# Optimization experiments

Hardware: AMD Instinct MI355X
Metric: run time of the kernel (lower is better)

## Reference

```python
import jax, jax.numpy as jnp
import numpy as np

LOSS_WEIGHT = 1.0
RADIUS = 1
DILATION = 2

def _mind_shift_indices():
    # six-neighbourhood offsets in a 3x3x3 kernel (as in torch code)
    six = np.array([[0, 1, 1], [1, 1, 0], [1, 0, 1], [1, 1, 2], [2, 1, 1], [1, 2, 1]])
    dist = ((six[:, None, :] - six[None, :, :]) ** 2).sum(-1)
    x, y = np.meshgrid(np.arange(6), np.arange(6), indexing='ij')
    mask = ((x > y) & (dist == 2)).reshape(-1)
    idx1 = np.repeat(six, 6, axis=0)[mask]
    idx2 = np.tile(six, (6, 1))[mask]
    return idx1, idx2

_IDX1, _IDX2 = _mind_shift_indices()

def _shifted(padded, idx, d, D, H, W):
    # one-hot dilated conv == static slice of replication-padded volume
    outs = [padded[:, :, a * d:a * d + D, b * d:b * d + H, c * d:c * d + W]
            for (a, b, c) in idx]
    return jnp.concatenate(outs, axis=1)  # (N, 12, D, H, W)

def mind_ssc(img, radius=RADIUS, dilation=DILATION):
    N, C, D, H, W = img.shape
    p = dilation
    padded = jnp.pad(img, ((0, 0), (0, 0), (p, p), (p, p), (p, p)), mode='edge')
    diff2 = (_shifted(padded, _IDX1, dilation, D, H, W)
             - _shifted(padded, _IDX2, dilation, D, H, W)) ** 2
    r = radius
    k = 2 * r + 1
    diff2p = jnp.pad(diff2, ((0, 0), (0, 0), (r, r), (r, r), (r, r)), mode='edge')
    ssd = jax.lax.reduce_window(diff2p, 0.0, jax.lax.add,
                                (1, 1, k, k, k), (1, 1, 1, 1, 1), 'VALID') / (k ** 3)
    mind = ssd - jnp.min(ssd, axis=1, keepdims=True)
    mind_var = jnp.mean(mind, axis=1, keepdims=True)
    m = jax.lax.stop_gradient(jnp.mean(mind_var))  # torch uses .item() -> detached
    mind_var = jnp.clip(mind_var, m * 0.001, m * 1000.0)
    return jnp.exp(-mind / mind_var)

def setup_inputs() -> dict:
    key = jax.random.key(0)
    k1, k2 = jax.random.split(key)
    shape = (2, 1, 128, 128, 128)
    predict = jax.random.normal(k1, shape, dtype=jnp.float32)
    target = jax.random.normal(k2, shape, dtype=jnp.float32)
    return {"predict": predict, "target": target}

def reference(predict, target):
    loss = jnp.mean((mind_ssc(predict) - mind_ssc(target)) ** 2)
    return loss * LOSS_WEIGHT
```

## Files before the change

kernel.cpp:

```cpp
#include <hip/hip_runtime.h>


#define DIM 128
#define HW (128 * 128)
#define DHW (128 * 128 * 128)
#define NVOX (2 * DHW)
#define LOSS_COUNT (2.0 * 12.0 * DHW)

#define TS   16
#define SY   18
#define NSP  (SY * TS)
#define CHZ  16
#define PSTR 7

typedef float f4 __attribute__((ext_vector_type(4)));
typedef float f2 __attribute__((ext_vector_type(2)));

__device__ __forceinline__ int clampi(int v) {
    v = v < 0 ? 0 : v;
    return v > 127 ? 127 : v;
}

__device__ __forceinline__ unsigned fkey(float f) {
    unsigned u = __float_as_uint(f);
    return (u & 0x80000000u) ? ~u : (u | 0x80000000u);
}
__device__ __forceinline__ float fdec(unsigned k) {
    unsigned u = (k & 0x80000000u) ? (k ^ 0x80000000u) : ~k;
    return __uint_as_float(u);
}

__device__ __forceinline__ void block_reduce_atomic(float v, double* dst) {
#pragma unroll
    for (int off = 32; off > 0; off >>= 1)
        v += __shfl_down(v, off, 64);
    __shared__ float red[4];
    int lane = threadIdx.x & 63;
    int wid  = threadIdx.x >> 6;
    if (lane == 0) red[wid] = v;
    __syncthreads();
    if (threadIdx.x == 0) {
        double t = (double)red[0] + (double)red[1] + (double)red[2] + (double)red[3];
        atomicAdd(dst, t);
    }
    __syncthreads();
}

__device__ __forceinline__ void block_minmax_atomic(float mnp, float mxp,
                                                    float mnt, float mxt,
                                                    unsigned* keys) {
#pragma unroll
    for (int off = 32; off > 0; off >>= 1) {
        mnp = fminf(mnp, __shfl_down(mnp, off, 64));
        mxp = fmaxf(mxp, __shfl_down(mxp, off, 64));
        mnt = fminf(mnt, __shfl_down(mnt, off, 64));
        mxt = fmaxf(mxt, __shfl_down(mxt, off, 64));
    }
    __shared__ float r[4][4];
    int lane = threadIdx.x & 63, wid = threadIdx.x >> 6;
    if (lane == 0) { r[wid][0] = mnp; r[wid][1] = mxp; r[wid][2] = mnt; r[wid][3] = mxt; }
    __syncthreads();
    if (threadIdx.x == 0) {
        float a = fminf(fminf(r[0][0], r[1][0]), fminf(r[2][0], r[3][0]));
        float b = fmaxf(fmaxf(r[0][1], r[1][1]), fmaxf(r[2][1], r[3][1]));
        float c = fminf(fminf(r[0][2], r[1][2]), fminf(r[2][2], r[3][2]));
        float d = fmaxf(fmaxf(r[0][3], r[1][3]), fmaxf(r[2][3], r[3][3]));
        atomicMin(&keys[0], fkey(a));
        atomicMax(&keys[1], fkey(b));
        atomicMin(&keys[2], fkey(c));
        atomicMax(&keys[3], fkey(d));
    }
    __syncthreads();
}

struct SPos {
    int y0, ym, yp;
    int cx[3], cm[3], cp[3];
    int woff;
};

__device__ __forceinline__ SPos make_spos(int p, int y0t, int x0t, int stride) {
    SPos q;
    int py = p >> 4, px = p & 15;
    int gy = clampi(y0t - 1 + py);
    int gx = x0t + px;
    q.y0 = gy * DIM; q.ym = clampi(gy - 2) * DIM; q.yp = clampi(gy + 2) * DIM;
#pragma unroll
    for (int wx = 0; wx < 3; ++wx) {
        int c = clampi(gx + wx - 1);
        q.cx[wx] = c;
        q.cm[wx] = clampi(c - 2);
        q.cp[wx] = clampi(c + 2);
    }
    q.woff = p * stride;
    return q;
}


__device__ __forceinline__ void stage_pair(const float* __restrict__ ip,
                                           const float* __restrict__ tp,
                                           int zm, int zc, int zp,
                                           const SPos& q, f4* __restrict__ X) {
    f2 acc[12];
#pragma unroll
    for (int c = 0; c < 12; ++c) acc[c] = (f2)0.0f;
#pragma unroll
    for (int wx = 0; wx < 3; ++wx) {
        int o0 = zm + q.y0 + q.cx[wx];
        int o1 = zc + q.y0 + q.cm[wx];
        int o2 = zc + q.ym + q.cx[wx];
        int o3 = zc + q.y0 + q.cp[wx];
        int o4 = zp + q.y0 + q.cx[wx];
        int o5 = zc + q.yp + q.cx[wx];
        f2 s0 = {ip[o0], tp[o0]};
        f2 s1 = {ip[o1], tp[o1]};
        f2 s2 = {ip[o2], tp[o2]};
        f2 s3 = {ip[o3], tp[o3]};
        f2 s4 = {ip[o4], tp[o4]};
        f2 s5 = {ip[o5], tp[o5]};
        f2 d;
        d = s1 - s0; acc[0]  += d * d;
        d = s2 - s0; acc[1]  += d * d;
        d = s2 - s1; acc[2]  += d * d;
        d = s3 - s0; acc[3]  += d * d;
        d = s3 - s2; acc[4]  += d * d;
        d = s4 - s1; acc[5]  += d * d;
        d = s4 - s2; acc[6]  += d * d;
        d = s4 - s3; acc[7]  += d * d;
        d = s5 - s0; acc[8]  += d * d;
        d = s5 - s1; acc[9]  += d * d;
        d = s5 - s3; acc[10] += d * d;
        d = s5 - s4; acc[11] += d * d;
    }
#pragma unroll
    for (int k = 0; k < 6; ++k) {
        f4 w;
        w.x = acc[2 * k].x;     w.y = acc[2 * k].y;
        w.z = acc[2 * k + 1].x; w.w = acc[2 * k + 1].y;
        X[q.woff + k] = w;
    }
}

__device__ __forceinline__ void box3y_pair(const f4* __restrict__ X,
                                           int ty, int tx, f4 q[6]) {
    int b0 = ((ty + 0) * TS + tx) * PSTR;
    int b1 = ((ty + 1) * TS + tx) * PSTR;
    int b2 = ((ty + 2) * TS + tx) * PSTR;
#pragma unroll
    for (int k = 0; k < 6; ++k)
        q[k] = X[b0 + k] + X[b1 + k] + X[b2 + k];
}

__global__ __launch_bounds__(256, 4) void fused_kernel(const float* __restrict__ pred,
                                                       const float* __restrict__ targ,
                                                       double* __restrict__ acc,
                                                       unsigned* __restrict__ keys) {
    __shared__ f4 X[NSP * PSTR];
    const int t = threadIdx.x;
    const int tile = blockIdx.x & 63, n = blockIdx.x >> 6;
    const int x0t = (tile & 7) * TS, y0t = (tile >> 3) * TS;
    const int z0 = blockIdx.y * CHZ;
    const float* ip = pred + (size_t)n * DHW;
    const float* tp = targ + (size_t)n * DHW;

    SPos pa = make_spos(t, y0t, x0t, PSTR);
    const bool hasB = (t + 256) < NSP;
    SPos pb = make_spos(hasB ? (t + 256) : 0, y0t, x0t, PSTR);

    const int ty = t >> 4, tx = t & 15;

    f4 A[6], B[6];
#pragma unroll
    for (int k = 0; k < 6; ++k) { A[k] = (f4)0.0f; B[k] = (f4)0.0f; }

    float vsump = 0.0f, vsumt = 0.0f, lsum = 0.0f;
    float locmnp = 1e30f, locmxp = -1e30f, locmnt = 1e30f, locmxt = -1e30f;

    for (int tz = z0 - 1; tz <= z0 + CHZ; ++tz) {
        int zq = clampi(tz);
        int zc = zq * HW, zm = clampi(zq - 2) * HW, zp = clampi(zq + 2) * HW;
        stage_pair(ip, tp, zm, zc, zp, pa, X);
        if (hasB) stage_pair(ip, tp, zm, zc, zp, pb, X);
        __syncthreads();

        f4 q[6];
        box3y_pair(X, ty, tx, q);
        __syncthreads();

        int ze = tz - 1;
        if (ze >= z0) {
            f4 v[6];
#pragma unroll
            for (int k = 0; k < 6; ++k) v[k] = A[k] + q[k];

            float mnp = v[0][0], mnt = v[0][1];
            float smp = 0.0f, smt = 0.0f;
#pragma unroll
            for (int c = 0; c < 12; ++c) {
                float pv = v[c >> 1][(c & 1) * 2];
                float tv = v[c >> 1][(c & 1) * 2 + 1];
                mnp = fminf(mnp, pv); smp += pv;
                mnt = fminf(mnt, tv); smt += tv;
            }
            float varp = smp * (1.0f / 12.0f) - mnp;
            float vart = smt * (1.0f / 12.0f) - mnt;
            vsump += varp; vsumt += vart;
            locmnp = fminf(locmnp, varp); locmxp = fmaxf(locmxp, varp);
            locmnt = fminf(locmnt, vart); locmxt = fmaxf(locmxt, vart);

            float invp = -1.0f / varp;
            float invt = -1.0f / vart;
            float la = 0.0f;
#pragma unroll
            for (int c = 0; c < 12; ++c) {
                float pv = v[c >> 1][(c & 1) * 2];
                float tv = v[c >> 1][(c & 1) * 2 + 1];
                float ep = __expf((pv - mnp) * invp);
                float et = __expf((tv - mnt) * invt);
                float dd = ep - et;
                la += dd * dd;
            }
            lsum += la;
        }
#pragma unroll
        for (int k = 0; k < 6; ++k) { A[k] = B[k] + q[k]; B[k] = q[k]; }
    }

    block_reduce_atomic(vsump, &acc[0]);
    block_reduce_atomic(vsumt, &acc[1]);
    block_reduce_atomic(lsum,  &acc[2]);
    block_minmax_atomic(locmnp, locmxp, locmnt, locmxt, keys);
}


__global__ void init_kernel(double* __restrict__ acc, unsigned* __restrict__ keys) {
    acc[0] = 0.0; acc[1] = 0.0; acc[2] = 0.0; acc[3] = 0.0;
    keys[0] = 0xFFFFFFFFu; keys[1] = 0u;
    keys[2] = 0xFFFFFFFFu; keys[3] = 0u;
    keys[4] = 0u;
}

__global__ void flag_kernel(const double* __restrict__ acc, unsigned* __restrict__ keys) {
    float m_p = (float)(acc[0] * (1.0 / (double)NVOX));
    float m_t = (float)(acc[1] * (1.0 / (double)NVOX));
    float mnp = fdec(keys[0]), mxp = fdec(keys[1]);
    float mnt = fdec(keys[2]), mxt = fdec(keys[3]);
    bool clean = (mnp >= m_p * 0.001f) && (mxp <= m_p * 1000.0f) &&
                 (mnt >= m_t * 0.001f) && (mxt <= m_t * 1000.0f);
    keys[4] = clean ? 0u : 1u;
}

__device__ __forceinline__ void stage_xsum(const float* __restrict__ im,
                                           int zm, int zc, int zp,
                                           const SPos& q, f4* __restrict__ P) {
    f4 a = (f4)0.0f, b = (f4)0.0f, c = (f4)0.0f;
#pragma unroll
    for (int wx = 0; wx < 3; ++wx) {
        float s0 = im[zm + q.y0 + q.cx[wx]];
        float s1 = im[zc + q.y0 + q.cm[wx]];
        float s2 = im[zc + q.ym + q.cx[wx]];
        float s3 = im[zc + q.y0 + q.cp[wx]];
        float s4 = im[zp + q.y0 + q.cx[wx]];
        float s5 = im[zc + q.yp + q.cx[wx]];
        float d;
        d = s1 - s0; a.x += d * d;
        d = s2 - s0; a.y += d * d;
        d = s2 - s1; a.z += d * d;
        d = s3 - s0; a.w += d * d;
        d = s3 - s2; b.x += d * d;
        d = s4 - s1; b.y += d * d;
        d = s4 - s2; b.z += d * d;
        d = s4 - s3; b.w += d * d;
        d = s5 - s0; c.x += d * d;
        d = s5 - s1; c.y += d * d;
        d = s5 - s3; c.z += d * d;
        d = s5 - s4; c.w += d * d;
    }
    P[q.woff + 0] = a;
    P[q.woff + 1] = b;
    P[q.woff + 2] = c;
}

__device__ __forceinline__ void box3y(const f4* __restrict__ P,
                                      int ty, int tx, f4 q[3]) {
    int base = (ty * TS + tx) * 3;
#pragma unroll
    for (int k = 0; k < 3; ++k)
        q[k] = P[base + k] + P[base + TS * 3 + k] + P[base + 2 * TS * 3 + k];
}

__device__ __forceinline__ float min12(const f4 v[3]) {
    float mn = v[0][0];
#pragma unroll
    for (int i = 0; i < 4; ++i)
        mn = fminf(mn, fminf(v[0][i], fminf(v[1][i], v[2][i])));
    return mn;
}
__device__ __forceinline__ float sum12(const f4 v[3]) {
    float sm = 0.0f;
#pragma unroll
    for (int i = 0; i < 4; ++i)
        sm += v[0][i] + v[1][i] + v[2][i];
    return sm;
}

__global__ __launch_bounds__(256, 4) void loss_kernel(const float* __restrict__ pred,
                                                      const float* __restrict__ targ,
                                                      const double* __restrict__ acc,
                                                      const unsigned* __restrict__ keys,
                                                      double* __restrict__ loss_sum) {
    if (keys[4] == 0u) return;

    __shared__ f4 Xp[NSP * 3];
    __shared__ f4 Xt[NSP * 3];
    const int t = threadIdx.x;
    const int tile = blockIdx.x & 63, n = blockIdx.x >> 6;
    const int x0t = (tile & 7) * TS, y0t = (tile >> 3) * TS;
    const int z0 = blockIdx.y * CHZ;
    const float* ip = pred + (size_t)n * DHW;
    const float* tp = targ + (size_t)n * DHW;

    const float m_p = (float)(acc[0] * (1.0 / (double)NVOX));
    const float m_t = (float)(acc[1] * (1.0 / (double)NVOX));

    SPos pa = make_spos(t, y0t, x0t, 3);
    const bool hasB = (t + 256) < NSP;
    SPos pb = make_spos(hasB ? (t + 256) : 0, y0t, x0t, 3);

    const int ty = t >> 4, tx = t & 15;

    f4 Ap[3], Bp[3], At[3], Bt[3];
#pragma unroll
    for (int q = 0; q < 3; ++q) {
        Ap[q] = (f4)0.0f; Bp[q] = (f4)0.0f;
        At[q] = (f4)0.0f; Bt[q] = (f4)0.0f;
    }
    float lsum = 0.0f;

    for (int tz = z0 - 1; tz <= z0 + CHZ; ++tz) {
        int zq = clampi(tz);
        int zc = zq * HW, zm = clampi(zq - 2) * HW, zp = clampi(zq + 2) * HW;
        stage_xsum(ip, zm, zc, zp, pa, Xp);
        stage_xsum(tp, zm, zc, zp, pa, Xt);
        if (hasB) {
            stage_xsum(ip, zm, zc, zp, pb, Xp);
            stage_xsum(tp, zm, zc, zp, pb, Xt);
        }
        __syncthreads();

        f4 qp[3], qt[3];
        box3y(Xp, ty, tx, qp);
        box3y(Xt, ty, tx, qt);
        __syncthreads();

        int ze = tz - 1;
        if (ze >= z0) {
            f4 vp[3], vt[3];
#pragma unroll
            for (int q = 0; q < 3; ++q) {
                vp[q] = Ap[q] + qp[q];
                vt[q] = At[q] + qt[q];
            }
            float mnp = min12(vp), smp = sum12(vp);
            float mnt = min12(vt), smt = sum12(vt);
            float varp = smp * (1.0f / 12.0f) - mnp;
            varp = fminf(fmaxf(varp, m_p * 0.001f), m_p * 1000.0f);
            float invp = -1.0f / varp;
            float vart = smt * (1.0f / 12.0f) - mnt;
            vart = fminf(fmaxf(vart, m_t * 0.001f), m_t * 1000.0f);
            float invt = -1.0f / vart;

            float a = 0.0f;
#pragma unroll
            for (int q = 0; q < 3; ++q)
#pragma unroll
                for (int i = 0; i < 4; ++i) {
                    float ep = __expf((vp[q][i] - mnp) * invp);
                    float et = __expf((vt[q][i] - mnt) * invt);
                    float dd = ep - et;
                    a += dd * dd;
                }
            lsum += a;
        }
#pragma unroll
        for (int q = 0; q < 3; ++q) {
            Ap[q] = Bp[q] + qp[q]; Bp[q] = qp[q];
            At[q] = Bt[q] + qt[q]; Bt[q] = qt[q];
        }
    }

    block_reduce_atomic(lsum, loss_sum);
}

__global__ void finalize_kernel(const double* __restrict__ acc,
                                const unsigned* __restrict__ keys,
                                float* __restrict__ out) {
    double l = (keys[4] == 0u) ? acc[2] : acc[3];
    out[0] = (float)(l * (1.0 / LOSS_COUNT));
}

extern "C" void kernel_launch(void* const* d_in, const int* in_sizes, int n_in,
                              void* d_out, int out_size, void* d_ws, size_t ws_size,
                              hipStream_t stream) {
    const float* pred = (const float*)d_in[0];
    const float* targ = (const float*)d_in[1];
    float* out = (float*)d_out;
    double* acc = (double*)d_ws;
    unsigned* keys = (unsigned*)((char*)d_ws + 64);

    dim3 block(256);
    dim3 grid(128, 8);

    init_kernel<<<1, 1, 0, stream>>>(acc, keys);
    fused_kernel<<<grid, block, 0, stream>>>(pred, targ, acc, keys);
    flag_kernel<<<1, 1, 0, stream>>>(acc, keys);
    loss_kernel<<<grid, block, 0, stream>>>(pred, targ, acc, keys, &acc[3]);
    finalize_kernel<<<1, 1, 0, stream>>>(acc, keys, out);
}
```

Baseline: 167.0 us.

## Fold init, flag and finalize kernels into memset and loss kernel

```diff
diff --git a/kernel.cpp b/kernel.cpp
--- a/kernel.cpp
+++ b/kernel.cpp
@@ -12,9 +12,11 @@
 #define NSP  (SY * TS)
 #define CHZ  16
 #define PSTR 7
+#define NBLK 1024
 
 typedef float f4 __attribute__((ext_vector_type(4)));
 typedef float f2 __attribute__((ext_vector_type(2)));
+
 
 __device__ __forceinline__ int clampi(int v) {
     v = v < 0 ? 0 : v;
@@ -65,10 +67,10 @@
         float b = fmaxf(fmaxf(r[0][1], r[1][1]), fmaxf(r[2][1], r[3][1]));
         float c = fminf(fminf(r[0][2], r[1][2]), fminf(r[2][2], r[3][2]));
         float d = fmaxf(fmaxf(r[0][3], r[1][3]), fmaxf(r[2][3], r[3][3]));
-        atomicMin(&keys[0], fkey(a));
-        atomicMax(&keys[1], fkey(b));
-        atomicMin(&keys[2], fkey(c));
-        atomicMax(&keys[3], fkey(d));
+        atomicMax(&keys[0], ~fkey(a));
+        atomicMax(&keys[1],  fkey(b));
+        atomicMax(&keys[2], ~fkey(c));
+        atomicMax(&keys[3],  fkey(d));
     }
     __syncthreads();
 }
@@ -96,22 +98,23 @@
     return q;
 }
 
-
 __device__ __forceinline__ void stage_pair(const float* __restrict__ ip,
                                            const float* __restrict__ tp,
                                            int zm, int zc, int zp,
                                            const SPos& q, f4* __restrict__ X) {
+    const int r0 = zm + q.y0, r1 = zc + q.y0, r2 = zc + q.ym;
+    const int r3 = zc + q.yp, r4 = zp + q.y0;
     f2 acc[12];
 #pragma unroll
     for (int c = 0; c < 12; ++c) acc[c] = (f2)0.0f;
 #pragma unroll
     for (int wx = 0; wx < 3; ++wx) {
-        int o0 = zm + q.y0 + q.cx[wx];
-        int o1 = zc + q.y0 + q.cm[wx];
-        int o2 = zc + q.ym + q.cx[wx];
-        int o3 = zc + q.y0 + q.cp[wx];
-        int o4 = zp + q.y0 + q.cx[wx];
-        int o5 = zc + q.yp + q.cx[wx];
+        int o0 = r0 + q.cx[wx];
+        int o1 = r1 + q.cm[wx];
+        int o2 = r2 + q.cx[wx];
+        int o3 = r1 + q.cp[wx];
+        int o4 = r4 + q.cx[wx];
+        int o5 = r3 + q.cx[wx];
         f2 s0 = {ip[o0], tp[o0]};
         f2 s1 = {ip[o1], tp[o1]};
         f2 s2 = {ip[o2], tp[o2]};
@@ -151,117 +154,20 @@
         q[k] = X[b0 + k] + X[b1 + k] + X[b2 + k];
 }
 
-__global__ __launch_bounds__(256, 4) void fused_kernel(const float* __restrict__ pred,
-                                                       const float* __restrict__ targ,
-                                                       double* __restrict__ acc,
-                                                       unsigned* __restrict__ keys) {
-    __shared__ f4 X[NSP * PSTR];
-    const int t = threadIdx.x;
-    const int tile = blockIdx.x & 63, n = blockIdx.x >> 6;
-    const int x0t = (tile & 7) * TS, y0t = (tile >> 3) * TS;
-    const int z0 = blockIdx.y * CHZ;
-    const float* ip = pred + (size_t)n * DHW;
-    const float* tp = targ + (size_t)n * DHW;
-
-    SPos pa = make_spos(t, y0t, x0t, PSTR);
-    const bool hasB = (t + 256) < NSP;
-    SPos pb = make_spos(hasB ? (t + 256) : 0, y0t, x0t, PSTR);
-
-    const int ty = t >> 4, tx = t & 15;
-
-    f4 A[6], B[6];
-#pragma unroll
-    for (int k = 0; k < 6; ++k) { A[k] = (f4)0.0f; B[k] = (f4)0.0f; }
-
-    float vsump = 0.0f, vsumt = 0.0f, lsum = 0.0f;
-    float locmnp = 1e30f, locmxp = -1e30f, locmnt = 1e30f, locmxt = -1e30f;
-
-    for (int tz = z0 - 1; tz <= z0 + CHZ; ++tz) {
-        int zq = clampi(tz);
-        int zc = zq * HW, zm = clampi(zq - 2) * HW, zp = clampi(zq + 2) * HW;
-        stage_pair(ip, tp, zm, zc, zp, pa, X);
-        if (hasB) stage_pair(ip, tp, zm, zc, zp, pb, X);
-        __syncthreads();
-
-        f4 q[6];
-        box3y_pair(X, ty, tx, q);
-        __syncthreads();
-
-        int ze = tz - 1;
-        if (ze >= z0) {
-            f4 v[6];
-#pragma unroll
-            for (int k = 0; k < 6; ++k) v[k] = A[k] + q[k];
-
-            float mnp = v[0][0], mnt = v[0][1];
-            float smp = 0.0f, smt = 0.0f;
-#pragma unroll
-            for (int c = 0; c < 12; ++c) {
-                float pv = v[c >> 1][(c & 1) * 2];
-                float tv = v[c >> 1][(c & 1) * 2 + 1];
-                mnp = fminf(mnp, pv); smp += pv;
-                mnt = fminf(mnt, tv); smt += tv;
-            }
-            float varp = smp * (1.0f / 12.0f) - mnp;
-            float vart = smt * (1.0f / 12.0f) - mnt;
-            vsump += varp; vsumt += vart;
-            locmnp = fminf(locmnp, varp); locmxp = fmaxf(locmxp, varp);
-            locmnt = fminf(locmnt, vart); locmxt = fmaxf(locmxt, vart);
-
-            float invp = -1.0f / varp;
-            float invt = -1.0f / vart;
-            float la = 0.0f;
-#pragma unroll
-            for (int c = 0; c < 12; ++c) {
-                float pv = v[c >> 1][(c & 1) * 2];
-                float tv = v[c >> 1][(c & 1) * 2 + 1];
-                float ep = __expf((pv - mnp) * invp);
-                float et = __expf((tv - mnt) * invt);
-                float dd = ep - et;
-                la += dd * dd;
-            }
-            lsum += la;
-        }
-#pragma unroll
-        for (int k = 0; k < 6; ++k) { A[k] = B[k] + q[k]; B[k] = q[k]; }
-    }
-
-    block_reduce_atomic(vsump, &acc[0]);
-    block_reduce_atomic(vsumt, &acc[1]);
-    block_reduce_atomic(lsum,  &acc[2]);
-    block_minmax_atomic(locmnp, locmxp, locmnt, locmxt, keys);
-}
-
-
-__global__ void init_kernel(double* __restrict__ acc, unsigned* __restrict__ keys) {
-    acc[0] = 0.0; acc[1] = 0.0; acc[2] = 0.0; acc[3] = 0.0;
-    keys[0] = 0xFFFFFFFFu; keys[1] = 0u;
-    keys[2] = 0xFFFFFFFFu; keys[3] = 0u;
-    keys[4] = 0u;
-}
-
-__global__ void flag_kernel(const double* __restrict__ acc, unsigned* __restrict__ keys) {
-    float m_p = (float)(acc[0] * (1.0 / (double)NVOX));
-    float m_t = (float)(acc[1] * (1.0 / (double)NVOX));
-    float mnp = fdec(keys[0]), mxp = fdec(keys[1]);
-    float mnt = fdec(keys[2]), mxt = fdec(keys[3]);
-    bool clean = (mnp >= m_p * 0.001f) && (mxp <= m_p * 1000.0f) &&
-                 (mnt >= m_t * 0.001f) && (mxt <= m_t * 1000.0f);
-    keys[4] = clean ? 0u : 1u;
-}
-
 __device__ __forceinline__ void stage_xsum(const float* __restrict__ im,
                                            int zm, int zc, int zp,
                                            const SPos& q, f4* __restrict__ P) {
+    const int r0 = zm + q.y0, r1 = zc + q.y0, r2 = zc + q.ym;
+    const int r3 = zc + q.yp, r4 = zp + q.y0;
     f4 a = (f4)0.0f, b = (f4)0.0f, c = (f4)0.0f;
 #pragma unroll
     for (int wx = 0; wx < 3; ++wx) {
-        float s0 = im[zm + q.y0 + q.cx[wx]];
-        float s1 = im[zc + q.y0 + q.cm[wx]];
-        float s2 = im[zc + q.ym + q.cx[wx]];
-        float s3 = im[zc + q.y0 + q.cp[wx]];
-        float s4 = im[zp + q.y0 + q.cx[wx]];
-        float s5 = im[zc + q.yp + q.cx[wx]];
+        float s0 = im[r0 + q.cx[wx]];
+        float s1 = im[r1 + q.cm[wx]];
+        float s2 = im[r2 + q.cx[wx]];
+        float s3 = im[r1 + q.cp[wx]];
+        float s4 = im[r4 + q.cx[wx]];
+        float s5 = im[r3 + q.cx[wx]];
         float d;
         d = s1 - s0; a.x += d * d;
         d = s2 - s0; a.y += d * d;
@@ -304,15 +210,13 @@
     return sm;
 }
 
-__global__ __launch_bounds__(256, 4) void loss_kernel(const float* __restrict__ pred,
-                                                      const float* __restrict__ targ,
-                                                      const double* __restrict__ acc,
-                                                      const unsigned* __restrict__ keys,
-                                                      double* __restrict__ loss_sum) {
-    if (keys[4] == 0u) return;
-
-    __shared__ f4 Xp[NSP * 3];
-    __shared__ f4 Xt[NSP * 3];
+
+__global__ __launch_bounds__(256, 4) void fused_kernel(const float* __restrict__ pred,
+                                                       const float* __restrict__ targ,
+                                                       double* __restrict__ acc,
+                                                       unsigned* __restrict__ keys) {
+    __shared__ f4 X[NSP * PSTR];
+
     const int t = threadIdx.x;
     const int tile = blockIdx.x & 63, n = blockIdx.x >> 6;
     const int x0t = (tile & 7) * TS, y0t = (tile >> 3) * TS;
@@ -320,13 +224,112 @@
     const float* ip = pred + (size_t)n * DHW;
     const float* tp = targ + (size_t)n * DHW;
 
-    const float m_p = (float)(acc[0] * (1.0 / (double)NVOX));
-    const float m_t = (float)(acc[1] * (1.0 / (double)NVOX));
+    SPos pa = make_spos(t, y0t, x0t, PSTR);
+    const bool hasB = (t + 256) < NSP;
+    SPos pb = make_spos(hasB ? (t + 256) : 0, y0t, x0t, PSTR);
+    const int ty = t >> 4, tx = t & 15;
+
+    f4 A[6], B[6];
+#pragma unroll
+    for (int k = 0; k < 6; ++k) { A[k] = (f4)0.0f; B[k] = (f4)0.0f; }
+
+    float vsump = 0.0f, vsumt = 0.0f, lsum = 0.0f;
+    float locmnp = 1e30f, locmxp = -1e30f, locmnt = 1e30f, locmxt = -1e30f;
+
+    for (int tz = z0 - 1; tz <= z0 + CHZ; ++tz) {
+        int zq = clampi(tz);
+        int zc = zq * HW, zm = clampi(zq - 2) * HW, zp = clampi(zq + 2) * HW;
+        stage_pair(ip, tp, zm, zc, zp, pa, X);
+        if (hasB) stage_pair(ip, tp, zm, zc, zp, pb, X);
+        __syncthreads();
+
+        f4 q[6];
+        box3y_pair(X, ty, tx, q);
+        __syncthreads();
+
+        int ze = tz - 1;
+        if (ze >= z0) {
+            f4 v[6];
+#pragma unroll
+            for (int k = 0; k < 6; ++k) v[k] = A[k] + q[k];
+
+            f2 sm2 = (f2)0.0f;
+            float mnp = v[0][0], mnt = v[0][1];
+#pragma unroll
+            for (int k = 0; k < 6; ++k) {
+                f2 a = {v[k].x, v[k].y};
+                f2 b = {v[k].z, v[k].w};
+                sm2 += a + b;
+                mnp = fminf(mnp, fminf(v[k].x, v[k].z));
+                mnt = fminf(mnt, fminf(v[k].y, v[k].w));
+            }
+            f2 mn2 = {mnp, mnt};
+            f2 var2 = sm2 * (1.0f / 12.0f) - mn2;
+            vsump += var2.x; vsumt += var2.y;
+            locmnp = fminf(locmnp, var2.x); locmxp = fmaxf(locmxp, var2.x);
+            locmnt = fminf(locmnt, var2.y); locmxt = fmaxf(locmxt, var2.y);
+
+            f2 inv2 = {-1.0f / var2.x, -1.0f / var2.y};
+            float la = 0.0f;
+#pragma unroll
+            for (int k = 0; k < 6; ++k) {
+                f2 a = ({ f2 u = {v[k].x, v[k].y}; (u - mn2) * inv2; });
+                f2 b = ({ f2 u = {v[k].z, v[k].w}; (u - mn2) * inv2; });
+                float d0 = __expf(a.x) - __expf(a.y);
+                float d1 = __expf(b.x) - __expf(b.y);
+                la += d0 * d0 + d1 * d1;
+            }
+            lsum += la;
+        }
+#pragma unroll
+        for (int k = 0; k < 6; ++k) { A[k] = B[k] + q[k]; B[k] = q[k]; }
+    }
+
+    block_reduce_atomic(vsump, &acc[0]);
+    block_reduce_atomic(vsumt, &acc[1]);
+    block_reduce_atomic(lsum,  &acc[2]);
+    block_minmax_atomic(locmnp, locmxp, locmnt, locmxt, keys);
+}
+
+
+__global__ __launch_bounds__(256, 4) void loss_kernel(const float* __restrict__ pred,
+                                                      const float* __restrict__ targ,
+                                                      double* __restrict__ acc,
+                                                      unsigned* __restrict__ keys,
+                                                      float* __restrict__ out) {
+    __shared__ float s_m[2];
+    __shared__ int s_clean;
+    const int t = threadIdx.x;
+    if (t == 0) {
+        float m_p = (float)(acc[0] * (1.0 / (double)NVOX));
+        float m_t = (float)(acc[1] * (1.0 / (double)NVOX));
+        float mnp = fdec(~keys[0]), mxp = fdec(keys[1]);
+        float mnt = fdec(~keys[2]), mxt = fdec(keys[3]);
+        bool clean = (mnp >= m_p * 0.001f) && (mxp <= m_p * 1000.0f) &&
+                     (mnt >= m_t * 0.001f) && (mxt <= m_t * 1000.0f);
+        s_m[0] = m_p; s_m[1] = m_t; s_clean = clean ? 1 : 0;
+    }
+    __syncthreads();
+
+    if (s_clean) {
+        if (blockIdx.x == 0 && blockIdx.y == 0 && t == 0)
+            out[0] = (float)(acc[2] * (1.0 / LOSS_COUNT));
+        return;
+    }
+
+    const float m_p = s_m[0], m_t = s_m[1];
+
+    __shared__ f4 Xp[NSP * 3];
+    __shared__ f4 Xt[NSP * 3];
+    const int tile = blockIdx.x & 63, n = blockIdx.x >> 6;
+    const int x0t = (tile & 7) * TS, y0t = (tile >> 3) * TS;
+    const int z0 = blockIdx.y * CHZ;
+    const float* ip = pred + (size_t)n * DHW;
+    const float* tp = targ + (size_t)n * DHW;
 
     SPos pa = make_spos(t, y0t, x0t, 3);
     const bool hasB = (t + 256) < NSP;
     SPos pb = make_spos(hasB ? (t + 256) : 0, y0t, x0t, 3);
-
     const int ty = t >> 4, tx = t & 15;
 
     f4 Ap[3], Bp[3], At[3], Bt[3];
@@ -389,14 +392,23 @@
         }
     }
 
-    block_reduce_atomic(lsum, loss_sum);
-}
-
-__global__ void finalize_kernel(const double* __restrict__ acc,
-                                const unsigned* __restrict__ keys,
-                                float* __restrict__ out) {
-    double l = (keys[4] == 0u) ? acc[2] : acc[3];
-    out[0] = (float)(l * (1.0 / LOSS_COUNT));
+#pragma unroll
+    for (int off = 32; off > 0; off >>= 1)
+        lsum += __shfl_down(lsum, off, 64);
+    __shared__ float red[4];
+    int lane = t & 63, wid = t >> 6;
+    if (lane == 0) red[wid] = lsum;
+    __syncthreads();
+    if (t == 0) {
+        double tt = (double)red[0] + red[1] + red[2] + red[3];
+        atomicAdd(&acc[3], tt);
+        unsigned old = atomicAdd(&keys[4], 1u);
+        if (old == NBLK - 1) {
+            double l = __hip_atomic_load(&acc[3], __ATOMIC_RELAXED,
+                                         __HIP_MEMORY_SCOPE_AGENT);
+            out[0] = (float)(l * (1.0 / LOSS_COUNT));
+        }
+    }
 }
 
 extern "C" void kernel_launch(void* const* d_in, const int* in_sizes, int n_in,
@@ -408,12 +420,10 @@
     double* acc = (double*)d_ws;
     unsigned* keys = (unsigned*)((char*)d_ws + 64);
 
+    hipMemsetAsync(d_ws, 0, 96, stream);
+
     dim3 block(256);
     dim3 grid(128, 8);
-
-    init_kernel<<<1, 1, 0, stream>>>(acc, keys);
     fused_kernel<<<grid, block, 0, stream>>>(pred, targ, acc, keys);
-    flag_kernel<<<1, 1, 0, stream>>>(acc, keys);
-    loss_kernel<<<grid, block, 0, stream>>>(pred, targ, acc, keys, &acc[3]);
-    finalize_kernel<<<1, 1, 0, stream>>>(acc, keys, out);
-}
+    loss_kernel<<<grid, block, 0, stream>>>(pred, targ, acc, keys, out);
+}
```

New measurement: 169.9 us. Within noise of the previous version (+1.7%).
